# Kernel optimization log

Measured on AMD Instinct MI355X. Metric: run time of the kernel, lower is better.

Reference implementation:

```python
import jax, jax.numpy as jnp
import numpy as np

LN_EPS = 1e-5


def _gather(x, idx):
    # x: [B, N, C], idx: [B, N, K] -> [B, N, K, C]
    return jax.vmap(lambda xb, ib: xb[ib])(x, idx)


def setup_inputs() -> dict:
    key = jax.random.key(0)
    ks = jax.random.split(key, 8)
    B, N, K, C_in, C_out, GEO = 2, 16384, 32, 128, 128, 10
    return {
        "points": jax.random.normal(ks[0], (B, N, 3), dtype=jnp.float32),
        "features": jax.random.normal(ks[1], (B, N, C_in), dtype=jnp.float32),
        "grouped_idx": jax.random.randint(ks[2], (B, N, K), 0, N, dtype=jnp.int32),
        "w_pos": jax.random.normal(ks[3], (GEO, C_in), dtype=jnp.float32) * (GEO ** -0.5),
        "b_pos": jnp.zeros((C_in,), jnp.float32),
        "w_gcm": jax.random.normal(ks[4], (C_in, C_in), dtype=jnp.float32) * (C_in ** -0.5),
        "b_gcm": jnp.zeros((C_in,), jnp.float32),
        "w_out": jax.random.normal(ks[5], (C_in, C_out), dtype=jnp.float32) * (C_in ** -0.5),
        "b_out": jnp.zeros((C_out,), jnp.float32),
        "ln_g": jnp.ones((C_out,), jnp.float32),
        "ln_b": jnp.zeros((C_out,), jnp.float32),
    }


def reference(points, features, grouped_idx, w_pos, b_pos, w_gcm, b_gcm,
              w_out, b_out, ln_g, ln_b):
    # gather neighbor coords and features: [B, N, K, *]
    grouped_pts = _gather(points, grouped_idx)
    xyz = points[..., 0:3]                      # [B, N, 3]
    grouped_xyz = grouped_pts[..., 0:3]         # [B, N, K, 3]
    center = xyz[:, :, None, :]                 # [B, N, 1, 3]
    diff = grouped_xyz - center                 # xi - xj
    dist = jnp.linalg.norm(diff, axis=-1, keepdims=True)  # ||xi - xj||
    K = grouped_xyz.shape[2]
    geo = jnp.concatenate(
        [jnp.broadcast_to(center, grouped_xyz.shape), grouped_xyz, diff, dist],
        axis=-1)                                # [B, N, K, 10]
    expanded_f = geo @ w_pos + b_pos            # pos_proj -> [B, N, K, C_in]
    grouped_f = _gather(features, grouped_idx)  # [B, N, K, C_in]
    h = jax.nn.relu((grouped_f + expanded_f) @ w_gcm + b_gcm)  # gcm_layer
    pooled = jnp.max(h, axis=2)                 # maxpooling over neighbors
    res = pooled + features                     # residual
    o = res @ w_out + b_out                     # out Linear
    mu = jnp.mean(o, axis=-1, keepdims=True)
    var = jnp.mean((o - mu) ** 2, axis=-1, keepdims=True)
    o = (o - mu) * jax.lax.rsqrt(var + LN_EPS) * ln_g + ln_b  # LayerNorm
    return jax.nn.relu(o)
```

## Files before the change

kernel.cpp:

```cpp
#include <hip/hip_runtime.h>
#include <hip/hip_bf16.h>
#include <math.h>

typedef __attribute__((ext_vector_type(8))) short short8;
typedef __attribute__((ext_vector_type(4))) short short4v;
typedef __attribute__((ext_vector_type(4))) float float4v;
typedef unsigned short ushort_t;

constexpr int NPTS = 32768;
constexpr int NN   = 16384;
constexpr int KK   = 32;
constexpr int CC   = 128;
constexpr int GRP  = 16;
constexpr int SG   = 40;
constexpr int SR   = 132;
#define LN_EPS 1e-5f

constexpr size_t WS_WP   = 0;
constexpr size_t WS_WO   = 40960;
constexpr size_t WS_BE   = 73728;
constexpr size_t WS_FB   = 79360;
constexpr size_t WS_NEED = WS_FB + (size_t)NPTS * CC * 2;

__device__ __forceinline__ short f2bs(float x) {
    return (short)__builtin_bit_cast(unsigned short, __float2bfloat16(x));
}
__device__ __forceinline__ float bs2f(ushort_t u) {
    return __uint_as_float(((unsigned)u) << 16);
}

__global__ __launch_bounds__(256) void prep_all(
    const float* __restrict__ features,
    const float* __restrict__ w_pos, const float* __restrict__ b_pos,
    const float* __restrict__ w_gcm, const float* __restrict__ b_gcm,
    const float* __restrict__ w_out,
    short* __restrict__ wsWp, short* __restrict__ wsWo, float* __restrict__ wsBeff,
    ushort_t* __restrict__ featbf, int do_convert)
{
    __shared__ float sPG[10 * 128];
    const int t = threadIdx.x, blk = blockIdx.x;

    if (blk < 512) {
        if (!do_convert) return;
        const int base = blk * 2048 + t;
        #pragma unroll
        for (int i = 0; i < 8; ++i) {
            const int f4 = base + i * 256;
            const float4 a = ((const float4*)features)[f4];
            short4v v; v[0]=f2bs(a.x); v[1]=f2bs(a.y); v[2]=f2bs(a.z); v[3]=f2bs(a.w);
            ((short4v*)featbf)[f4] = v;
        }
        return;
    }
    if (blk == 512) {
        #pragma unroll 4
        for (int e = t; e < 16 * 128 * 8; e += 256) {
            const int j = e & 7, n = (e >> 3) & 127, g = e >> 10;
            wsWp[e] = f2bs(w_gcm[(g * 8 + j) * 128 + n]);
        }
        return;
    }
    if (blk == 513) {
        const int c = t & 127, half = t >> 7;
        for (int gi = 0; gi < 5; ++gi) {
            const int g = gi * 2 + half;
            float s = 0.f;
            #pragma unroll
            for (int r = 0; r < 128; ++r) s += w_pos[g * 128 + r] * w_gcm[r * 128 + c];
            sPG[g * 128 + c] = s;
        }
        if (t < 128) {
            float s = b_gcm[t];
            #pragma unroll
            for (int r = 0; r < 128; ++r) s += b_pos[r] * w_gcm[r * 128 + t];
            wsBeff[t] = s;
        }
        __syncthreads();
        #pragma unroll 4
        for (int e2 = t; e2 < 4 * 128 * 8; e2 += 256) {
            const int e = 16 * 128 * 8 + e2;
            const int j = e & 7, n = (e >> 3) & 127, g = e >> 10;
            const int k = g * 8 + j;
            wsWp[e] = (k < 138) ? f2bs(sPG[(k - 128) * 128 + n]) : (short)0;
        }
        return;
    }
    #pragma unroll 4
    for (int e = t; e < 128 * 128; e += 256) {
        const int j = e & 7, n = (e >> 3) & 127, g = e >> 10;
        wsWo[e] = f2bs(w_out[(g * 8 + j) * 128 + n]);
    }
}

template<int DMA>
__global__ __launch_bounds__(256) void bridge_main(
    const float* __restrict__ points, const float* __restrict__ features,
    const int*   __restrict__ gidx,
    const short* __restrict__ wsWp, const short* __restrict__ wsWo,
    const float* __restrict__ wsBeff, const ushort_t* __restrict__ featbf,
    const float* __restrict__ b_out, const float* __restrict__ ln_g,
    const float* __restrict__ ln_b,
    float* __restrict__ out)
{
    __shared__ short sA[2][KK * CC];
    __shared__ short sG[2][KK * SG];
    __shared__ short sRes[GRP * SR];
    __shared__ ushort_t sIdx[GRP * KK];

    float* sPS = (float*)&sG[0][0];
    float* sPQ = sPS + 4 * GRP;

    const int t = threadIdx.x, wv = t >> 6, lane = t & 63;
    const int quad = (t >> 4) & 3, m = t & 15;
    const int g0 = blockIdx.x * GRP;
    const int nbase = (g0 >= NN) ? NN : 0;
    const int col0 = wv * 32 + m;

    sIdx[t]       = (ushort_t)gidx[(size_t)g0 * KK + t];
    sIdx[t + 256] = (ushort_t)gidx[(size_t)g0 * KK + t + 256];
    if (t < 128) {
        const int b = t >> 6, r = (t >> 1) & 31, h = t & 1;
        *(short8*)&sG[b][r * SG + 16 + h * 8] = (short8)0;
    }

    short8 bWp[5][2];
    #pragma unroll
    for (int ks = 0; ks < 5; ++ks)
        #pragma unroll
        for (int ntl = 0; ntl < 2; ++ntl)
            bWp[ks][ntl] = *((const short8*)wsWp + ((ks * 4 + quad) * 128 + col0 + ntl * 16));
    float beffv[2] = { wsBeff[col0], wsBeff[col0 + 16] };

    __syncthreads();

    const int r0 = wv * 4 + (lane >> 4);
    const int pc = lane & 15;
    const int gc = pc ^ r0;

    float4 ff0a, ff0b, ff1a, ff1b;
    float gcx, gcy, gcz, ggx, ggy, ggz;

    auto issue_dma = [&](int p, int buf) {
        const int kn0 = nbase + sIdx[p * KK + r0];
        const int kn1 = nbase + sIdx[p * KK + r0 + 16];
        const ushort_t* gp0 = featbf + (size_t)kn0 * CC + gc * 8;
        const ushort_t* gp1 = featbf + (size_t)kn1 * CC + gc * 8;
        short* l0 = &sA[buf][(wv * 4) * CC];
        short* l1 = &sA[buf][(wv * 4 + 16) * CC];
        __builtin_amdgcn_global_load_lds((const __attribute__((address_space(1))) void*)gp0,
                                         (__attribute__((address_space(3))) void*)l0, 16, 0, 0);
        __builtin_amdgcn_global_load_lds((const __attribute__((address_space(1))) void*)gp1,
                                         (__attribute__((address_space(3))) void*)l1, 16, 0, 0);
    };
    auto fb_load = [&](int p) {
        const int kn0 = nbase + sIdx[p * KK + r0];
        const int kn1 = nbase + sIdx[p * KK + r0 + 16];
        const float4* f0 = (const float4*)(features + (size_t)kn0 * CC + gc * 8);
        const float4* f1 = (const float4*)(features + (size_t)kn1 * CC + gc * 8);
        ff0a = f0[0]; ff0b = f0[1]; ff1a = f1[0]; ff1b = f1[1];
    };
    auto fb_store = [&](int buf) {
        short8 v;
        v[0]=f2bs(ff0a.x); v[1]=f2bs(ff0a.y); v[2]=f2bs(ff0a.z); v[3]=f2bs(ff0a.w);
        v[4]=f2bs(ff0b.x); v[5]=f2bs(ff0b.y); v[6]=f2bs(ff0b.z); v[7]=f2bs(ff0b.w);
        *(short8*)&sA[buf][r0 * CC + pc * 8] = v;
        v[0]=f2bs(ff1a.x); v[1]=f2bs(ff1a.y); v[2]=f2bs(ff1a.z); v[3]=f2bs(ff1a.w);
        v[4]=f2bs(ff1b.x); v[5]=f2bs(ff1b.y); v[6]=f2bs(ff1b.z); v[7]=f2bs(ff1b.w);
        *(short8*)&sA[buf][(r0 + 16) * CC + pc * 8] = v;
    };
    auto geo_load = [&](int p) {
        if (lane < 8) {
            const int j  = wv * 8 + lane;
            const int pt = g0 + p;
            const int kn = nbase + sIdx[p * KK + j];
            gcx = points[(size_t)pt * 3 + 0]; gcy = points[(size_t)pt * 3 + 1]; gcz = points[(size_t)pt * 3 + 2];
            ggx = points[(size_t)kn * 3 + 0]; ggy = points[(size_t)kn * 3 + 1]; ggz = points[(size_t)kn * 3 + 2];
        }
    };
    auto geo_store = [&](int buf) {
        if (lane < 8) {
            const int j = wv * 8 + lane;
            const float dx = ggx - gcx, dy = ggy - gcy, dz = ggz - gcz;
            const float dist = sqrtf(dx * dx + dy * dy + dz * dz);
            short8 v0, v1 = (short8)0;
            v0[0]=f2bs(gcx); v0[1]=f2bs(gcy); v0[2]=f2bs(gcz);
            v0[3]=f2bs(ggx); v0[4]=f2bs(ggy); v0[5]=f2bs(ggz);
            v0[6]=f2bs(dx);  v0[7]=f2bs(dy);
            v1[0]=f2bs(dz);  v1[1]=f2bs(dist);
            *(short8*)&sG[buf][j * SG + 0] = v0;
            *(short8*)&sG[buf][j * SG + 8] = v1;
        }
    };

    if constexpr (DMA) issue_dma(0, 0); else fb_load(0);
    geo_load(0);
    if constexpr (!DMA) fb_store(0);
    geo_store(0);
    __syncthreads();

    int offA[4];
    #pragma unroll
    for (int ks = 0; ks < 4; ++ks) offA[ks] = m * CC + (((ks * 4 + quad) ^ m) * 8);
    const int offG = m * SG + quad * 8;

    for (int p = 0; p < GRP; ++p) {
        const int buf = p & 1, nbuf = buf ^ 1;
        if (p + 1 < GRP) {
            if constexpr (DMA) issue_dma(p + 1, nbuf); else fb_load(p + 1);
            geo_load(p + 1);
        }

        const short* ab = sA[buf];
        const short* ag = sG[buf];
        float4v acc[2][2] = {};
        #pragma unroll
        for (int ks = 0; ks < 4; ++ks) {
            const short8 a0 = *(const short8*)(ab + offA[ks]);
            const short8 a1 = *(const short8*)(ab + offA[ks] + 16 * CC);
            acc[0][0] = __builtin_amdgcn_mfma_f32_16x16x32_bf16(a0, bWp[ks][0], acc[0][0], 0, 0, 0);
            acc[0][1] = __builtin_amdgcn_mfma_f32_16x16x32_bf16(a0, bWp[ks][1], acc[0][1], 0, 0, 0);
            acc[1][0] = __builtin_amdgcn_mfma_f32_16x16x32_bf16(a1, bWp[ks][0], acc[1][0], 0, 0, 0);
            acc[1][1] = __builtin_amdgcn_mfma_f32_16x16x32_bf16(a1, bWp[ks][1], acc[1][1], 0, 0, 0);
        }
        {
            const short8 a0 = *(const short8*)(ag + offG);
            const short8 a1 = *(const short8*)(ag + offG + 16 * SG);
            acc[0][0] = __builtin_amdgcn_mfma_f32_16x16x32_bf16(a0, bWp[4][0], acc[0][0], 0, 0, 0);
            acc[0][1] = __builtin_amdgcn_mfma_f32_16x16x32_bf16(a0, bWp[4][1], acc[0][1], 0, 0, 0);
            acc[1][0] = __builtin_amdgcn_mfma_f32_16x16x32_bf16(a1, bWp[4][0], acc[1][0], 0, 0, 0);
            acc[1][1] = __builtin_amdgcn_mfma_f32_16x16x32_bf16(a1, bWp[4][1], acc[1][1], 0, 0, 0);
        }

        if (p + 1 < GRP) {
            if constexpr (!DMA) fb_store(nbuf);
            geo_store(nbuf);
        }

        const int pt = g0 + p;
        #pragma unroll
        for (int ntl = 0; ntl < 2; ++ntl) {
            float v = acc[0][ntl][0];
            #pragma unroll
            for (int r = 1; r < 4; ++r) v = fmaxf(v, acc[0][ntl][r]);
            #pragma unroll
            for (int r = 0; r < 4; ++r) v = fmaxf(v, acc[1][ntl][r]);
            v = fmaxf(v, __shfl_xor(v, 16));
            v = fmaxf(v, __shfl_xor(v, 32));
            v = fmaxf(v + beffv[ntl], 0.f);
            float fc;
            if constexpr (DMA) fc = bs2f(featbf[(size_t)pt * CC + col0 + ntl * 16]);
            else               fc = features[(size_t)pt * CC + col0 + ntl * 16];
            const float res = v + fc;
            if (quad == 0) sRes[p * SR + col0 + ntl * 16] = f2bs(res);
        }
        __syncthreads();
    }

    short8 bWo[4][2];
    #pragma unroll
    for (int ks = 0; ks < 4; ++ks)
        #pragma unroll
        for (int ntl = 0; ntl < 2; ++ntl)
            bWo[ks][ntl] = *((const short8*)wsWo + ((ks * 4 + quad) * 128 + col0 + ntl * 16));

    const short* rm = sRes + m * SR;
    float4v acc2[2] = {};
    #pragma unroll
    for (int ks = 0; ks < 4; ++ks) {
        const short8 a = *(const short8*)(rm + ks * 32 + quad * 8);
        acc2[0] = __builtin_amdgcn_mfma_f32_16x16x32_bf16(a, bWo[ks][0], acc2[0], 0, 0, 0);
        acc2[1] = __builtin_amdgcn_mfma_f32_16x16x32_bf16(a, bWo[ks][1], acc2[1], 0, 0, 0);
    }

    const float boutv[2] = { b_out[col0], b_out[col0 + 16] };
    const float lngv[2]  = { ln_g[col0], ln_g[col0 + 16] };
    const float lnbv[2]  = { ln_b[col0], ln_b[col0 + 16] };

    #pragma unroll
    for (int r = 0; r < 4; ++r) {
        const float o0 = acc2[0][r] + boutv[0];
        const float o1 = acc2[1][r] + boutv[1];
        float ss = o0 + o1, qq = o0 * o0 + o1 * o1;
        #pragma unroll
        for (int d = 1; d < 16; d <<= 1) { ss += __shfl_xor(ss, d); qq += __shfl_xor(qq, d); }
        if (m == 0) { sPS[wv * GRP + quad * 4 + r] = ss; sPQ[wv * GRP + quad * 4 + r] = qq; }
    }
    __syncthreads();

    #pragma unroll
    for (int r = 0; r < 4; ++r) {
        const int R = quad * 4 + r;
        const float S = sPS[0 * GRP + R] + sPS[1 * GRP + R] + sPS[2 * GRP + R] + sPS[3 * GRP + R];
        const float Q = sPQ[0 * GRP + R] + sPQ[1 * GRP + R] + sPQ[2 * GRP + R] + sPQ[3 * GRP + R];
        const float mu  = S * (1.f / 128.f);
        const float var = fmaxf(Q * (1.f / 128.f) - mu * mu, 0.f);
        const float rstd = rsqrtf(var + LN_EPS);
        const float o0 = acc2[0][r] + boutv[0];
        const float o1 = acc2[1][r] + boutv[1];
        const size_t base = (size_t)(g0 + R) * CC;
        out[base + col0]      = fmaxf((o0 - mu) * rstd * lngv[0] + lnbv[0], 0.f);
        out[base + col0 + 16] = fmaxf((o1 - mu) * rstd * lngv[1] + lnbv[1], 0.f);
    }
}

extern "C" void kernel_launch(void* const* d_in, const int* in_sizes, int n_in,
                              void* d_out, int out_size, void* d_ws, size_t ws_size,
                              hipStream_t stream) {
    const float* points   = (const float*)d_in[0];
    const float* features = (const float*)d_in[1];
    const int*   gidx     = (const int*)  d_in[2];
    const float* w_pos    = (const float*)d_in[3];
    const float* b_pos    = (const float*)d_in[4];
    const float* w_gcm    = (const float*)d_in[5];
    const float* b_gcm    = (const float*)d_in[6];
    const float* w_out    = (const float*)d_in[7];
    const float* b_out    = (const float*)d_in[8];
    const float* ln_g     = (const float*)d_in[9];
    const float* ln_b     = (const float*)d_in[10];
    float* out = (float*)d_out;

    char* ws = (char*)d_ws;
    short*    wsWp   = (short*)(ws + WS_WP);
    short*    wsWo   = (short*)(ws + WS_WO);
    float*    wsBeff = (float*)(ws + WS_BE);
    ushort_t* featbf = (ushort_t*)(ws + WS_FB);

    const bool use_dma = (ws_size >= WS_NEED);

    hipLaunchKernelGGL(prep_all, dim3(515), dim3(256), 0, stream,
                       features, w_pos, b_pos, w_gcm, b_gcm, w_out,
                       wsWp, wsWo, wsBeff, featbf, use_dma ? 1 : 0);
    if (use_dma) {
        hipLaunchKernelGGL((bridge_main<1>), dim3(NPTS / GRP), dim3(256), 0, stream,
                           points, features, gidx, wsWp, wsWo, wsBeff, featbf,
                           b_out, ln_g, ln_b, out);
    } else {
        hipLaunchKernelGGL((bridge_main<0>), dim3(NPTS / GRP), dim3(256), 0, stream,
                           points, features, gidx, wsWp, wsWo, wsBeff, featbf,
                           b_out, ln_g, ln_b, out);
    }
}
```

Baseline: 167.6 us.

## Halve block to two waves and eight points, each wave covering 64 columns

The main kernel now uses 128-thread blocks that each process 8 center points instead of 16, launching twice as many blocks. Each wave computes 64 output columns with four MFMA tiles per row block, and each thread issues four row gathers per point. The LayerNorm reduction is reduced from four waves to two, and half of the residual tile is padded with zeros. The aim is more blocks in flight and more MFMA work per wave, at the cost of higher register pressure and reloading the weight fragments in twice as many blocks.

```diff
diff --git a/kernel.cpp b/kernel.cpp
--- a/kernel.cpp
+++ b/kernel.cpp
@@ -11,7 +11,7 @@
 constexpr int NN   = 16384;
 constexpr int KK   = 32;
 constexpr int CC   = 128;
-constexpr int GRP  = 16;
+constexpr int GRP  = 8;
 constexpr int SG   = 40;
 constexpr int SR   = 132;
 #define LN_EPS 1e-5f
@@ -93,7 +93,7 @@
 }
 
 template<int DMA>
-__global__ __launch_bounds__(256) void bridge_main(
+__global__ __launch_bounds__(128) void bridge_main(
     const float* __restrict__ points, const float* __restrict__ features,
     const int*   __restrict__ gidx,
     const short* __restrict__ wsWp, const short* __restrict__ wsWo,
@@ -104,73 +104,79 @@
 {
     __shared__ short sA[2][KK * CC];
     __shared__ short sG[2][KK * SG];
-    __shared__ short sRes[GRP * SR];
+    __shared__ short sRes[16 * SR];
     __shared__ ushort_t sIdx[GRP * KK];
 
     float* sPS = (float*)&sG[0][0];
-    float* sPQ = sPS + 4 * GRP;
+    float* sPQ = sPS + 2 * 16;
 
     const int t = threadIdx.x, wv = t >> 6, lane = t & 63;
     const int quad = (t >> 4) & 3, m = t & 15;
+    const int ch = wv;
     const int g0 = blockIdx.x * GRP;
     const int nbase = (g0 >= NN) ? NN : 0;
-    const int col0 = wv * 32 + m;
-
-    sIdx[t]       = (ushort_t)gidx[(size_t)g0 * KK + t];
-    sIdx[t + 256] = (ushort_t)gidx[(size_t)g0 * KK + t + 256];
-    if (t < 128) {
+
+    sIdx[t]         = (ushort_t)gidx[(size_t)g0 * KK + t];
+    sIdx[t + 128]   = (ushort_t)gidx[(size_t)g0 * KK + t + 128];
+    {
         const int b = t >> 6, r = (t >> 1) & 31, h = t & 1;
         *(short8*)&sG[b][r * SG + 16 + h * 8] = (short8)0;
     }
-
-    short8 bWp[5][2];
+    for (int e = t; e < 8 * SR; e += 128) sRes[8 * SR + e] = 0;
+
+    short8 bWp[5][4];
     #pragma unroll
     for (int ks = 0; ks < 5; ++ks)
         #pragma unroll
-        for (int ntl = 0; ntl < 2; ++ntl)
-            bWp[ks][ntl] = *((const short8*)wsWp + ((ks * 4 + quad) * 128 + col0 + ntl * 16));
-    float beffv[2] = { wsBeff[col0], wsBeff[col0 + 16] };
+        for (int n = 0; n < 4; ++n)
+            bWp[ks][n] = ((const short8*)wsWp)[(ks * 4 + quad) * 128 + ch * 64 + n * 16 + m];
+    float beffv[4];
+    #pragma unroll
+    for (int n = 0; n < 4; ++n) beffv[n] = wsBeff[ch * 64 + n * 16 + m];
 
     __syncthreads();
 
-    const int r0 = wv * 4 + (lane >> 4);
-    const int pc = lane & 15;
-    const int gc = pc ^ r0;
-
-    float4 ff0a, ff0b, ff1a, ff1b;
+    const int rsub = lane >> 4;
+    const int pc   = lane & 15;
+
+    float4 fb0[4], fb1[4];
     float gcx, gcy, gcz, ggx, ggy, ggz;
 
     auto issue_dma = [&](int p, int buf) {
-        const int kn0 = nbase + sIdx[p * KK + r0];
-        const int kn1 = nbase + sIdx[p * KK + r0 + 16];
-        const ushort_t* gp0 = featbf + (size_t)kn0 * CC + gc * 8;
-        const ushort_t* gp1 = featbf + (size_t)kn1 * CC + gc * 8;
-        short* l0 = &sA[buf][(wv * 4) * CC];
-        short* l1 = &sA[buf][(wv * 4 + 16) * CC];
-        __builtin_amdgcn_global_load_lds((const __attribute__((address_space(1))) void*)gp0,
-                                         (__attribute__((address_space(3))) void*)l0, 16, 0, 0);
-        __builtin_amdgcn_global_load_lds((const __attribute__((address_space(1))) void*)gp1,
-                                         (__attribute__((address_space(3))) void*)l1, 16, 0, 0);
+        #pragma unroll
+        for (int i = 0; i < 4; ++i) {
+            const int row = i * 8 + wv * 4 + rsub;
+            const int gc  = pc ^ (row & 15);
+            const int kn  = nbase + sIdx[p * KK + row];
+            const ushort_t* gp = featbf + (size_t)kn * CC + gc * 8;
+            short* lp = &sA[buf][(i * 8 + wv * 4) * CC];
+            __builtin_amdgcn_global_load_lds((const __attribute__((address_space(1))) void*)gp,
+                                             (__attribute__((address_space(3))) void*)lp, 16, 0, 0);
+        }
     };
     auto fb_load = [&](int p) {
-        const int kn0 = nbase + sIdx[p * KK + r0];
-        const int kn1 = nbase + sIdx[p * KK + r0 + 16];
-        const float4* f0 = (const float4*)(features + (size_t)kn0 * CC + gc * 8);
-        const float4* f1 = (const float4*)(features + (size_t)kn1 * CC + gc * 8);
-        ff0a = f0[0]; ff0b = f0[1]; ff1a = f1[0]; ff1b = f1[1];
+        #pragma unroll
+        for (int i = 0; i < 4; ++i) {
+            const int row = i * 8 + wv * 4 + rsub;
+            const int gc  = pc ^ (row & 15);
+            const int kn  = nbase + sIdx[p * KK + row];
+            const float4* fp = (const float4*)(features + (size_t)kn * CC + gc * 8);
+            fb0[i] = fp[0]; fb1[i] = fp[1];
+        }
     };
     auto fb_store = [&](int buf) {
-        short8 v;
-        v[0]=f2bs(ff0a.x); v[1]=f2bs(ff0a.y); v[2]=f2bs(ff0a.z); v[3]=f2bs(ff0a.w);
-        v[4]=f2bs(ff0b.x); v[5]=f2bs(ff0b.y); v[6]=f2bs(ff0b.z); v[7]=f2bs(ff0b.w);
-        *(short8*)&sA[buf][r0 * CC + pc * 8] = v;
-        v[0]=f2bs(ff1a.x); v[1]=f2bs(ff1a.y); v[2]=f2bs(ff1a.z); v[3]=f2bs(ff1a.w);
-        v[4]=f2bs(ff1b.x); v[5]=f2bs(ff1b.y); v[6]=f2bs(ff1b.z); v[7]=f2bs(ff1b.w);
-        *(short8*)&sA[buf][(r0 + 16) * CC + pc * 8] = v;
+        #pragma unroll
+        for (int i = 0; i < 4; ++i) {
+            const int row = i * 8 + wv * 4 + rsub;
+            short8 v;
+            v[0]=f2bs(fb0[i].x); v[1]=f2bs(fb0[i].y); v[2]=f2bs(fb0[i].z); v[3]=f2bs(fb0[i].w);
+            v[4]=f2bs(fb1[i].x); v[5]=f2bs(fb1[i].y); v[6]=f2bs(fb1[i].z); v[7]=f2bs(fb1[i].w);
+            *(short8*)&sA[buf][row * CC + pc * 8] = v;
+        }
     };
     auto geo_load = [&](int p) {
-        if (lane < 8) {
-            const int j  = wv * 8 + lane;
+        if (lane < 16) {
+            const int j  = wv * 16 + lane;
             const int pt = g0 + p;
             const int kn = nbase + sIdx[p * KK + j];
             gcx = points[(size_t)pt * 3 + 0]; gcy = points[(size_t)pt * 3 + 1]; gcz = points[(size_t)pt * 3 + 2];
@@ -178,8 +184,8 @@
         }
     };
     auto geo_store = [&](int buf) {
-        if (lane < 8) {
-            const int j = wv * 8 + lane;
+        if (lane < 16) {
+            const int j = wv * 16 + lane;
             const float dx = ggx - gcx, dy = ggy - gcy, dz = ggz - gcz;
             const float dist = sqrtf(dx * dx + dy * dy + dz * dz);
             short8 v0, v1 = (short8)0;
@@ -212,23 +218,25 @@
 
         const short* ab = sA[buf];
         const short* ag = sG[buf];
-        float4v acc[2][2] = {};
+        float4v acc[2][4] = {};
         #pragma unroll
         for (int ks = 0; ks < 4; ++ks) {
             const short8 a0 = *(const short8*)(ab + offA[ks]);
             const short8 a1 = *(const short8*)(ab + offA[ks] + 16 * CC);
-            acc[0][0] = __builtin_amdgcn_mfma_f32_16x16x32_bf16(a0, bWp[ks][0], acc[0][0], 0, 0, 0);
-            acc[0][1] = __builtin_amdgcn_mfma_f32_16x16x32_bf16(a0, bWp[ks][1], acc[0][1], 0, 0, 0);
-            acc[1][0] = __builtin_amdgcn_mfma_f32_16x16x32_bf16(a1, bWp[ks][0], acc[1][0], 0, 0, 0);
-            acc[1][1] = __builtin_amdgcn_mfma_f32_16x16x32_bf16(a1, bWp[ks][1], acc[1][1], 0, 0, 0);
+            #pragma unroll
+            for (int n = 0; n < 4; ++n) {
+                acc[0][n] = __builtin_amdgcn_mfma_f32_16x16x32_bf16(a0, bWp[ks][n], acc[0][n], 0, 0, 0);
+                acc[1][n] = __builtin_amdgcn_mfma_f32_16x16x32_bf16(a1, bWp[ks][n], acc[1][n], 0, 0, 0);
+            }
         }
         {
             const short8 a0 = *(const short8*)(ag + offG);
             const short8 a1 = *(const short8*)(ag + offG + 16 * SG);
-            acc[0][0] = __builtin_amdgcn_mfma_f32_16x16x32_bf16(a0, bWp[4][0], acc[0][0], 0, 0, 0);
-            acc[0][1] = __builtin_amdgcn_mfma_f32_16x16x32_bf16(a0, bWp[4][1], acc[0][1], 0, 0, 0);
-            acc[1][0] = __builtin_amdgcn_mfma_f32_16x16x32_bf16(a1, bWp[4][0], acc[1][0], 0, 0, 0);
-            acc[1][1] = __builtin_amdgcn_mfma_f32_16x16x32_bf16(a1, bWp[4][1], acc[1][1], 0, 0, 0);
+            #pragma unroll
+            for (int n = 0; n < 4; ++n) {
+                acc[0][n] = __builtin_amdgcn_mfma_f32_16x16x32_bf16(a0, bWp[4][n], acc[0][n], 0, 0, 0);
+                acc[1][n] = __builtin_amdgcn_mfma_f32_16x16x32_bf16(a1, bWp[4][n], acc[1][n], 0, 0, 0);
+            }
         }
 
         if (p + 1 < GRP) {
@@ -238,68 +246,78 @@
 
         const int pt = g0 + p;
         #pragma unroll
-        for (int ntl = 0; ntl < 2; ++ntl) {
-            float v = acc[0][ntl][0];
-            #pragma unroll
-            for (int r = 1; r < 4; ++r) v = fmaxf(v, acc[0][ntl][r]);
-            #pragma unroll
-            for (int r = 0; r < 4; ++r) v = fmaxf(v, acc[1][ntl][r]);
+        for (int n = 0; n < 4; ++n) {
+            float v = acc[0][n][0];
+            #pragma unroll
+            for (int r = 1; r < 4; ++r) v = fmaxf(v, acc[0][n][r]);
+            #pragma unroll
+            for (int r = 0; r < 4; ++r) v = fmaxf(v, acc[1][n][r]);
             v = fmaxf(v, __shfl_xor(v, 16));
             v = fmaxf(v, __shfl_xor(v, 32));
-            v = fmaxf(v + beffv[ntl], 0.f);
+            v = fmaxf(v + beffv[n], 0.f);
             float fc;
-            if constexpr (DMA) fc = bs2f(featbf[(size_t)pt * CC + col0 + ntl * 16]);
-            else               fc = features[(size_t)pt * CC + col0 + ntl * 16];
+            if constexpr (DMA) fc = bs2f(featbf[(size_t)pt * CC + ch * 64 + n * 16 + m]);
+            else               fc = features[(size_t)pt * CC + ch * 64 + n * 16 + m];
             const float res = v + fc;
-            if (quad == 0) sRes[p * SR + col0 + ntl * 16] = f2bs(res);
+            if (quad == 0) sRes[p * SR + ch * 64 + n * 16 + m] = f2bs(res);
         }
         __syncthreads();
     }
 
-    short8 bWo[4][2];
+    short8 bWo[4][4];
     #pragma unroll
     for (int ks = 0; ks < 4; ++ks)
         #pragma unroll
-        for (int ntl = 0; ntl < 2; ++ntl)
-            bWo[ks][ntl] = *((const short8*)wsWo + ((ks * 4 + quad) * 128 + col0 + ntl * 16));
+        for (int n = 0; n < 4; ++n)
+            bWo[ks][n] = ((const short8*)wsWo)[(ks * 4 + quad) * 128 + ch * 64 + n * 16 + m];
 
     const short* rm = sRes + m * SR;
-    float4v acc2[2] = {};
+    float4v acc2[4] = {};
     #pragma unroll
     for (int ks = 0; ks < 4; ++ks) {
-        const short8 a = *(const short8*)(rm + ks * 32 + quad * 8);
-        acc2[0] = __builtin_amdgcn_mfma_f32_16x16x32_bf16(a, bWo[ks][0], acc2[0], 0, 0, 0);
-        acc2[1] = __builtin_amdgcn_mfma_f32_16x16x32_bf16(a, bWo[ks][1], acc2[1], 0, 0, 0);
-    }
-
-    const float boutv[2] = { b_out[col0], b_out[col0 + 16] };
-    const float lngv[2]  = { ln_g[col0], ln_g[col0 + 16] };
-    const float lnbv[2]  = { ln_b[col0], ln_b[col0 + 16] };
+        const short8 a = *(const short8*)(rm + (ks * 4 + quad) * 8);
+        #pragma unroll
+        for (int n = 0; n < 4; ++n)
+            acc2[n] = __builtin_amdgcn_mfma_f32_16x16x32_bf16(a, bWo[ks][n], acc2[n], 0, 0, 0);
+    }
+
+    float boutv[4], lngv[4], lnbv[4];
+    #pragma unroll
+    for (int n = 0; n < 4; ++n) {
+        const int c = ch * 64 + n * 16 + m;
+        boutv[n] = b_out[c]; lngv[n] = ln_g[c]; lnbv[n] = ln_b[c];
+    }
 
     #pragma unroll
     for (int r = 0; r < 4; ++r) {
-        const float o0 = acc2[0][r] + boutv[0];
-        const float o1 = acc2[1][r] + boutv[1];
-        float ss = o0 + o1, qq = o0 * o0 + o1 * o1;
+        float ss = 0.f, qq = 0.f;
+        #pragma unroll
+        for (int n = 0; n < 4; ++n) {
+            const float o = acc2[n][r] + boutv[n];
+            ss += o; qq += o * o;
+        }
         #pragma unroll
         for (int d = 1; d < 16; d <<= 1) { ss += __shfl_xor(ss, d); qq += __shfl_xor(qq, d); }
-        if (m == 0) { sPS[wv * GRP + quad * 4 + r] = ss; sPQ[wv * GRP + quad * 4 + r] = qq; }
+        if (m == 0) { sPS[wv * 16 + quad * 4 + r] = ss; sPQ[wv * 16 + quad * 4 + r] = qq; }
     }
     __syncthreads();
 
     #pragma unroll
     for (int r = 0; r < 4; ++r) {
         const int R = quad * 4 + r;
-        const float S = sPS[0 * GRP + R] + sPS[1 * GRP + R] + sPS[2 * GRP + R] + sPS[3 * GRP + R];
-        const float Q = sPQ[0 * GRP + R] + sPQ[1 * GRP + R] + sPQ[2 * GRP + R] + sPQ[3 * GRP + R];
-        const float mu  = S * (1.f / 128.f);
-        const float var = fmaxf(Q * (1.f / 128.f) - mu * mu, 0.f);
-        const float rstd = rsqrtf(var + LN_EPS);
-        const float o0 = acc2[0][r] + boutv[0];
-        const float o1 = acc2[1][r] + boutv[1];
-        const size_t base = (size_t)(g0 + R) * CC;
-        out[base + col0]      = fmaxf((o0 - mu) * rstd * lngv[0] + lnbv[0], 0.f);
-        out[base + col0 + 16] = fmaxf((o1 - mu) * rstd * lngv[1] + lnbv[1], 0.f);
+        if (R < GRP) {
+            const float S = sPS[R] + sPS[16 + R];
+            const float Q = sPQ[R] + sPQ[16 + R];
+            const float mu  = S * (1.f / 128.f);
+            const float var = fmaxf(Q * (1.f / 128.f) - mu * mu, 0.f);
+            const float rstd = rsqrtf(var + LN_EPS);
+            const size_t base = (size_t)(g0 + R) * CC;
+            #pragma unroll
+            for (int n = 0; n < 4; ++n) {
+                const float o = acc2[n][r] + boutv[n];
+                out[base + ch * 64 + n * 16 + m] = fmaxf((o - mu) * rstd * lngv[n] + lnbv[n], 0.f);
+            }
+        }
     }
 }
 
@@ -331,11 +349,11 @@
                        features, w_pos, b_pos, w_gcm, b_gcm, w_out,
                        wsWp, wsWo, wsBeff, featbf, use_dma ? 1 : 0);
     if (use_dma) {
-        hipLaunchKernelGGL((bridge_main<1>), dim3(NPTS / GRP), dim3(256), 0, stream,
+        hipLaunchKernelGGL((bridge_main<1>), dim3(NPTS / GRP), dim3(128), 0, stream,
                            points, features, gidx, wsWp, wsWo, wsBeff, featbf,
                            b_out, ln_g, ln_b, out);
     } else {
-        hipLaunchKernelGGL((bridge_main<0>), dim3(NPTS / GRP), dim3(256), 0, stream,
+        hipLaunchKernelGGL((bridge_main<0>), dim3(NPTS / GRP), dim3(128), 0, stream,
                            points, features, gidx, wsWp, wsWo, wsBeff, featbf,
                            b_out, ln_g, ln_b, out);
     }
```

New measurement: 188.9 us. 12.7% more time.
